# Kernel optimization log

Measured on AMD Instinct MI355X. Metric: run time of the kernel, lower is better.

## Reference

```python
import jax, jax.numpy as jnp
import numpy as np
import math

H_SP, W_SP = 200, 200          # BEV spatial shape (single level, m == h)
D_MODEL = 256
N_HEADS = 8
N_POINTS = 4
D_HEAD = D_MODEL // N_HEADS


def _grid_init_bias():
    # Matches TemporalSelfAttention._reset_parameters for sampling_offsets.bias
    thetas = np.arange(N_HEADS, dtype=np.float32) * (2.0 * np.pi / N_HEADS)
    grid = np.stack([np.cos(thetas), np.sin(thetas)], -1)
    grid = grid / np.abs(grid).max(-1, keepdims=True)
    grid = np.tile(grid[:, None, None, :], (1, 1, N_POINTS, 1))  # (NH, 1, P, 2)
    for i in range(N_POINTS):
        grid[:, :, i, :] *= (i + 1)
    return jnp.asarray(grid.reshape(-1), dtype=jnp.float32)


def setup_inputs() -> dict:
    key = jax.random.key(0)
    ks = jax.random.split(key, 10)
    N = 1
    Lq = H_SP * W_SP
    Lin = H_SP * W_SP
    xav = math.sqrt(6.0 / (2 * D_MODEL))
    query = jax.random.normal(ks[0], (N, Lq, D_MODEL), jnp.float32)
    query_pos = jax.random.normal(ks[1], (N, Lq, D_MODEL), jnp.float32)
    reference_points = jax.random.uniform(ks[2], (N, Lq, 1, 2), jnp.float32)
    input_flatten = jax.random.normal(ks[3], (N, Lin, D_MODEL), jnp.float32)
    W_value = jax.random.uniform(ks[4], (D_MODEL, D_MODEL), jnp.float32, -xav, xav)
    b_value = jnp.zeros((D_MODEL,), jnp.float32)
    # small random weights (trained-model-like) + canonical grid bias
    W_off = jax.random.normal(ks[5], (N_HEADS * N_POINTS * 2, D_MODEL), jnp.float32) * 0.005
    b_off = _grid_init_bias()
    W_attn = jax.random.normal(ks[6], (N_HEADS * N_POINTS, D_MODEL), jnp.float32) * 0.02
    b_attn = jnp.zeros((N_HEADS * N_POINTS,), jnp.float32)
    W_out = jax.random.uniform(ks[7], (D_MODEL, D_MODEL), jnp.float32, -xav, xav)
    b_out = jnp.zeros((D_MODEL,), jnp.float32)
    return dict(query=query, query_pos=query_pos, reference_points=reference_points,
                input_flatten=input_flatten, W_value=W_value, b_value=b_value,
                W_off=W_off, b_off=b_off, W_attn=W_attn, b_attn=b_attn,
                W_out=W_out, b_out=b_out)


def _bilinear_sample(vflat, x, y):
    # vflat: (N, NH, H*W, DH); x, y: (N, NH, K) pixel coords (align_corners=False)
    # Zero padding outside the feature map, matching the MSDeformAttn CUDA kernel.
    x0f = jnp.floor(x)
    y0f = jnp.floor(y)
    x0 = x0f.astype(jnp.int32)
    y0 = y0f.astype(jnp.int32)
    lw = x - x0f
    lh = y - y0f
    gather = jax.vmap(jax.vmap(lambda v, i: v[i]))  # over batch, head
    acc = jnp.zeros(x.shape + (vflat.shape[-1],), vflat.dtype)
    corners = ((y0, x0, (1.0 - lh) * (1.0 - lw)),
               (y0, x0 + 1, (1.0 - lh) * lw),
               (y0 + 1, x0, lh * (1.0 - lw)),
               (y0 + 1, x0 + 1, lh * lw))
    for yi, xi, wgt in corners:
        valid = ((xi >= 0) & (xi < W_SP) & (yi >= 0) & (yi < H_SP)).astype(vflat.dtype)
        idx = jnp.clip(yi, 0, H_SP - 1) * W_SP + jnp.clip(xi, 0, W_SP - 1)
        g = gather(vflat, idx)                      # (N, NH, K, DH)
        acc = acc + (wgt * valid)[..., None] * g
    return acc


def reference(query, query_pos, reference_points, input_flatten,
              W_value, b_value, W_off, b_off, W_attn, b_attn, W_out, b_out):
    N, Lq, _ = query.shape
    q = query + query_pos
    value = input_flatten @ W_value.T + b_value                     # (N, Lin, D)
    value = value.reshape(N, -1, N_HEADS, D_HEAD).transpose(0, 2, 1, 3)  # (N, NH, Lin, DH)
    off = (q @ W_off.T + b_off).reshape(N, Lq, N_HEADS, N_POINTS, 2)
    attn = jax.nn.softmax((q @ W_attn.T + b_attn).reshape(N, Lq, N_HEADS, N_POINTS), axis=-1)
    norm = jnp.array([W_SP, H_SP], jnp.float32)                      # offset_normalizer (w, h)
    ref = reference_points[:, :, 0, :][:, :, None, None, :]          # (N, Lq, 1, 1, 2)
    loc = ref + off / norm                                           # (N, Lq, NH, P, 2) in [0,1]
    x = (loc[..., 0] * W_SP - 0.5).transpose(0, 2, 1, 3).reshape(N, N_HEADS, Lq * N_POINTS)
    y = (loc[..., 1] * H_SP - 0.5).transpose(0, 2, 1, 3).reshape(N, N_HEADS, Lq * N_POINTS)
    sampled = _bilinear_sample(value, x, y).reshape(N, N_HEADS, Lq, N_POINTS, D_HEAD)
    out = jnp.einsum('nhqpd,nqhp->nqhd', sampled, attn).reshape(N, Lq, D_MODEL)
    return out @ W_out.T + b_out
```

## Files before the change

kernel.cpp:

```cpp
#include <hip/hip_runtime.h>
#include <math.h>

#define LQ 40000
#define DMODEL 256
#define NHD 8
#define NPT 4
#define DHD 32
#define HSP 200
#define WSP 200

typedef short s16x8 __attribute__((ext_vector_type(8)));
typedef float f32x4 __attribute__((ext_vector_type(4)));

__device__ __forceinline__ unsigned short f2b(float f) {
    unsigned u = __builtin_bit_cast(unsigned, f);
    u += 0x7FFFu + ((u >> 16) & 1u);
    return (unsigned short)(u >> 16);
}
__device__ __forceinline__ float b2f(unsigned short u) {
    return __builtin_bit_cast(float, ((unsigned)u) << 16);
}

template <typename AT, typename CT, bool HasA2>
__global__ __launch_bounds__(256) void gemm_mfma(
    const AT* __restrict__ A, const float* __restrict__ A2,
    const float* __restrict__ W1, const float* __restrict__ b1,
    const float* __restrict__ W2, const float* __restrict__ b2,
    int split, int ncols, CT* __restrict__ C, int ldC)
{
    constexpr int LDA = 264;
    __shared__ __align__(16) unsigned short Asm[64 * LDA];
    __shared__ __align__(16) unsigned short Bsm[64 * LDA];

    const int t = threadIdx.x;
    const int rowBase = blockIdx.x * 64;
    const int colBase = blockIdx.y * 64;

#pragma unroll
    for (int rep = 0; rep < 8; ++rep) {
        int f8 = t + 256 * rep;
        int row = f8 >> 5;
        int c8 = f8 & 31;
        unsigned short* dst = &Asm[row * LDA + c8 * 8];
        if constexpr (sizeof(AT) == 4) {
            const float* Ap = (const float*)A + (size_t)(rowBase + row) * 256 + c8 * 8;
            float4 v0 = *(const float4*)Ap;
            float4 v1 = *(const float4*)(Ap + 4);
            if constexpr (HasA2) {
                const float* Bp = A2 + (size_t)(rowBase + row) * 256 + c8 * 8;
                float4 w0 = *(const float4*)Bp;
                float4 w1 = *(const float4*)(Bp + 4);
                v0.x += w0.x; v0.y += w0.y; v0.z += w0.z; v0.w += w0.w;
                v1.x += w1.x; v1.y += w1.y; v1.z += w1.z; v1.w += w1.w;
            }
            union { unsigned short u[8]; uint4 v; } tmp;
            tmp.u[0] = f2b(v0.x); tmp.u[1] = f2b(v0.y);
            tmp.u[2] = f2b(v0.z); tmp.u[3] = f2b(v0.w);
            tmp.u[4] = f2b(v1.x); tmp.u[5] = f2b(v1.y);
            tmp.u[6] = f2b(v1.z); tmp.u[7] = f2b(v1.w);
            *(uint4*)dst = tmp.v;
        } else {
            const unsigned short* Ap =
                (const unsigned short*)A + (size_t)(rowBase + row) * 256 + c8 * 8;
            *(uint4*)dst = *(const uint4*)Ap;
        }
    }

#pragma unroll
    for (int rep = 0; rep < 8; ++rep) {
        int f8 = t + 256 * rep;
        int row = f8 >> 5;
        int c8 = f8 & 31;
        int n = colBase + row;
        int nc = n < ncols ? n : (ncols - 1);
        const float* Wp = (nc < split) ? (W1 + (size_t)nc * 256)
                                       : (W2 + (size_t)(nc - split) * 256);
        float4 v0 = *(const float4*)(Wp + c8 * 8);
        float4 v1 = *(const float4*)(Wp + c8 * 8 + 4);
        union { unsigned short u[8]; uint4 v; } tmp;
        tmp.u[0] = f2b(v0.x); tmp.u[1] = f2b(v0.y);
        tmp.u[2] = f2b(v0.z); tmp.u[3] = f2b(v0.w);
        tmp.u[4] = f2b(v1.x); tmp.u[5] = f2b(v1.y);
        tmp.u[6] = f2b(v1.z); tmp.u[7] = f2b(v1.w);
        *(uint4*)&Bsm[row * LDA + c8 * 8] = tmp.v;
    }

    __syncthreads();

    const int wave = t >> 6;
    const int lane = t & 63;
    const int l15 = lane & 15;
    const int quad = lane >> 4;

    f32x4 acc[4];
#pragma unroll
    for (int m = 0; m < 4; ++m) acc[m] = (f32x4){0.f, 0.f, 0.f, 0.f};

#pragma unroll
    for (int ks = 0; ks < 8; ++ks) {
        s16x8 bfrag = *(const s16x8*)&Bsm[(wave * 16 + l15) * LDA + ks * 32 + quad * 8];
#pragma unroll
        for (int m = 0; m < 4; ++m) {
            s16x8 afrag = *(const s16x8*)&Asm[(m * 16 + l15) * LDA + ks * 32 + quad * 8];
            acc[m] = __builtin_amdgcn_mfma_f32_16x16x32_bf16(afrag, bfrag, acc[m], 0, 0, 0);
        }
    }

    const int col = colBase + wave * 16 + l15;
    if (col < ncols) {
        float bb = (col < split) ? b1[col] : b2[col - split];
#pragma unroll
        for (int m = 0; m < 4; ++m)
#pragma unroll
            for (int r2 = 0; r2 < 4; ++r2) {
                int row = rowBase + m * 16 + quad * 4 + r2;
                float v = acc[m][r2] + bb;
                if constexpr (sizeof(CT) == 2)
                    C[(size_t)row * ldC + col] = (CT)f2b(v);
                else
                    C[(size_t)row * ldC + col] = (CT)v;
            }
    }
}

__global__ __launch_bounds__(256) void sample_kernel(
    const float* __restrict__ raw, const float* __restrict__ rp,
    const unsigned short* __restrict__ value, unsigned short* __restrict__ outa)
{
    __shared__ int4   sIdx[8][8][4];
    __shared__ float4 sW[8][8][4];

    const int t = threadIdx.x;
    {
        const int qi = t >> 5, h = (t >> 2) & 7, p = t & 3;
        const int q = blockIdx.x * 8 + qi;
        const float* r = raw + (size_t)q * 96;
        float l0 = r[64 + h * 4 + 0], l1 = r[64 + h * 4 + 1];
        float l2 = r[64 + h * 4 + 2], l3 = r[64 + h * 4 + 3];
        float mx = fmaxf(fmaxf(l0, l1), fmaxf(l2, l3));
        float e0 = __expf(l0 - mx), e1 = __expf(l1 - mx);
        float e2 = __expf(l2 - mx), e3 = __expf(l3 - mx);
        float inv = 1.f / (e0 + e1 + e2 + e3);
        float ep = (p == 0) ? e0 : (p == 1) ? e1 : (p == 2) ? e2 : e3;
        float wp = ep * inv;

        float x = rp[(size_t)q * 2 + 0] * (float)WSP - 0.5f + r[h * 8 + p * 2 + 0];
        float y = rp[(size_t)q * 2 + 1] * (float)HSP - 0.5f + r[h * 8 + p * 2 + 1];
        float x0f = floorf(x), y0f = floorf(y);
        int x0 = (int)x0f, y0 = (int)y0f;
        float lw = x - x0f, lh = y - y0f;
        float cw[4] = {(1.f - lh) * (1.f - lw), (1.f - lh) * lw,
                       lh * (1.f - lw), lh * lw};
        int4 I; float4 W;
        int* Ip = &I.x; float* Wp = &W.x;
#pragma unroll
        for (int c = 0; c < 4; ++c) {
            int cx = x0 + (c & 1), cy = y0 + (c >> 1);
            bool valid = (cx >= 0) & (cx < WSP) & (cy >= 0) & (cy < HSP);
            int ccx = cx < 0 ? 0 : (cx > WSP - 1 ? WSP - 1 : cx);
            int ccy = cy < 0 ? 0 : (cy > HSP - 1 ? HSP - 1 : cy);
            Ip[c] = (ccy * WSP + ccx) * DMODEL + h * DHD;
            Wp[c] = valid ? cw[c] * wp : 0.f;
        }
        sIdx[qi][h][p] = I;
        sW[qi][h][p] = W;
    }
    __syncthreads();

    const int h = t >> 5, d = t & 31;
    for (int qi = 0; qi < 8; ++qi) {
        float acc = 0.f;
#pragma unroll
        for (int p = 0; p < 4; ++p) {
            int4 I = sIdx[qi][h][p];
            float4 W = sW[qi][h][p];
            acc += W.x * b2f(value[I.x + d]);
            acc += W.y * b2f(value[I.y + d]);
            acc += W.z * b2f(value[I.z + d]);
            acc += W.w * b2f(value[I.w + d]);
        }
        int q = blockIdx.x * 8 + qi;
        outa[(size_t)q * DMODEL + h * DHD + d] = f2b(acc);
    }
}

extern "C" void kernel_launch(void* const* d_in, const int* in_sizes, int n_in,
                              void* d_out, int out_size, void* d_ws, size_t ws_size,
                              hipStream_t stream)
{
    const float* query         = (const float*)d_in[0];
    const float* query_pos     = (const float*)d_in[1];
    const float* ref_points    = (const float*)d_in[2];
    const float* input_flatten = (const float*)d_in[3];
    const float* W_value       = (const float*)d_in[4];
    const float* b_value       = (const float*)d_in[5];
    const float* W_off         = (const float*)d_in[6];
    const float* b_off         = (const float*)d_in[7];
    const float* W_attn        = (const float*)d_in[8];
    const float* b_attn        = (const float*)d_in[9];
    const float* W_out         = (const float*)d_in[10];
    const float* b_out         = (const float*)d_in[11];
    float* out = (float*)d_out;

    unsigned short* val  = (unsigned short*)d_ws;
    float*          raw  = (float*)(val + (size_t)LQ * DMODEL);
    unsigned short* outa = (unsigned short*)(raw + (size_t)LQ * 96);

    dim3 blk(256);

    gemm_mfma<float, unsigned short, false><<<dim3(LQ / 64, 4), blk, 0, stream>>>(
        input_flatten, nullptr, W_value, b_value, W_value, b_value, 256, 256,
        val, DMODEL);

    gemm_mfma<float, float, true><<<dim3(LQ / 64, 2), blk, 0, stream>>>(
        query, query_pos, W_off, b_off, W_attn, b_attn, 64, 96, raw, 96);

    sample_kernel<<<dim3(LQ / 8), blk, 0, stream>>>(raw, ref_points, val, outa);

    gemm_mfma<unsigned short, float, false><<<dim3(LQ / 64, 4), blk, 0, stream>>>(
        outa, nullptr, W_out, b_out, W_out, b_out, 256, 256, out, DMODEL);
}
```

Baseline: 287.0 us.

## Pre-convert weights to bf16 and compute full output width per GEMM block

```diff
diff --git a/kernel.cpp b/kernel.cpp
--- a/kernel.cpp
+++ b/kernel.cpp
@@ -21,105 +21,127 @@
     return __builtin_bit_cast(float, ((unsigned)u) << 16);
 }
 
-template <typename AT, typename CT, bool HasA2>
+__global__ __launch_bounds__(256) void convert_weights(
+    const float* __restrict__ s0, const float* __restrict__ s1,
+    const float* __restrict__ s2, const float* __restrict__ s3,
+    unsigned short* __restrict__ dst)
+{
+    int i4 = (blockIdx.x * 256 + threadIdx.x) * 4;
+    const float* src;
+    int base;
+    if (i4 < 65536)       { src = s0; base = 0; }
+    else if (i4 < 81920)  { src = s1; base = 65536; }
+    else if (i4 < 90112)  { src = s2; base = 81920; }
+    else                  { src = s3; base = 90112; }
+    float4 v = *(const float4*)(src + (i4 - base));
+    union { unsigned short u[4]; uint2 q; } tmp;
+    tmp.u[0] = f2b(v.x); tmp.u[1] = f2b(v.y);
+    tmp.u[2] = f2b(v.z); tmp.u[3] = f2b(v.w);
+    *(uint2*)(dst + i4) = tmp.q;
+}
+
+template <int NCOLS, typename AT, typename CT, bool HasA2>
 __global__ __launch_bounds__(256) void gemm_mfma(
     const AT* __restrict__ A, const float* __restrict__ A2,
-    const float* __restrict__ W1, const float* __restrict__ b1,
-    const float* __restrict__ W2, const float* __restrict__ b2,
-    int split, int ncols, CT* __restrict__ C, int ldC)
-{
-    constexpr int LDA = 264;
-    __shared__ __align__(16) unsigned short Asm[64 * LDA];
-    __shared__ __align__(16) unsigned short Bsm[64 * LDA];
+    const unsigned short* __restrict__ Wb,
+    const float* __restrict__ b1, const float* __restrict__ b2, int split,
+    CT* __restrict__ C)
+{
+    constexpr int NT = NCOLS / 16;
+    constexpr int JMAX = (NT + 3) / 4;
+    constexpr int PITCH = 72;
+    __shared__ __align__(16) unsigned short As[64 * PITCH];
+    __shared__ __align__(16) unsigned short Bs[NCOLS * PITCH];
 
     const int t = threadIdx.x;
-    const int rowBase = blockIdx.x * 64;
-    const int colBase = blockIdx.y * 64;
-
-#pragma unroll
-    for (int rep = 0; rep < 8; ++rep) {
-        int f8 = t + 256 * rep;
-        int row = f8 >> 5;
-        int c8 = f8 & 31;
-        unsigned short* dst = &Asm[row * LDA + c8 * 8];
-        if constexpr (sizeof(AT) == 4) {
-            const float* Ap = (const float*)A + (size_t)(rowBase + row) * 256 + c8 * 8;
-            float4 v0 = *(const float4*)Ap;
-            float4 v1 = *(const float4*)(Ap + 4);
-            if constexpr (HasA2) {
-                const float* Bp = A2 + (size_t)(rowBase + row) * 256 + c8 * 8;
-                float4 w0 = *(const float4*)Bp;
-                float4 w1 = *(const float4*)(Bp + 4);
-                v0.x += w0.x; v0.y += w0.y; v0.z += w0.z; v0.w += w0.w;
-                v1.x += w1.x; v1.y += w1.y; v1.z += w1.z; v1.w += w1.w;
+    const int wave = t >> 6, lane = t & 63;
+    const int l15 = lane & 15, quad = lane >> 4;
+    const size_t rowBase = (size_t)blockIdx.x * 64;
+
+    f32x4 acc[4][JMAX];
+#pragma unroll
+    for (int m = 0; m < 4; ++m)
+#pragma unroll
+        for (int j = 0; j < JMAX; ++j) acc[m][j] = (f32x4){0.f, 0.f, 0.f, 0.f};
+
+    for (int k0 = 0; k0 < 256; k0 += 64) {
+        if (k0) __syncthreads();
+#pragma unroll
+        for (int rep = 0; rep < 2; ++rep) {
+            int f8 = t + 256 * rep;
+            int row = f8 >> 3, g = f8 & 7;
+            unsigned short* dst = &As[row * PITCH + g * 8];
+            if constexpr (sizeof(AT) == 4) {
+                const float* Ap = (const float*)A + (rowBase + row) * 256 + k0 + g * 8;
+                float4 v0 = *(const float4*)Ap;
+                float4 v1 = *(const float4*)(Ap + 4);
+                if constexpr (HasA2) {
+                    const float* Bp = A2 + (rowBase + row) * 256 + k0 + g * 8;
+                    float4 w0 = *(const float4*)Bp;
+                    float4 w1 = *(const float4*)(Bp + 4);
+                    v0.x += w0.x; v0.y += w0.y; v0.z += w0.z; v0.w += w0.w;
+                    v1.x += w1.x; v1.y += w1.y; v1.z += w1.z; v1.w += w1.w;
+                }
+                union { unsigned short u[8]; uint4 v; } tmp;
+                tmp.u[0] = f2b(v0.x); tmp.u[1] = f2b(v0.y);
+                tmp.u[2] = f2b(v0.z); tmp.u[3] = f2b(v0.w);
+                tmp.u[4] = f2b(v1.x); tmp.u[5] = f2b(v1.y);
+                tmp.u[6] = f2b(v1.z); tmp.u[7] = f2b(v1.w);
+                *(uint4*)dst = tmp.v;
+            } else {
+                const unsigned short* Ap =
+                    (const unsigned short*)A + (rowBase + row) * 256 + k0 + g * 8;
+                *(uint4*)dst = *(const uint4*)Ap;
             }
-            union { unsigned short u[8]; uint4 v; } tmp;
-            tmp.u[0] = f2b(v0.x); tmp.u[1] = f2b(v0.y);
-            tmp.u[2] = f2b(v0.z); tmp.u[3] = f2b(v0.w);
-            tmp.u[4] = f2b(v1.x); tmp.u[5] = f2b(v1.y);
-            tmp.u[6] = f2b(v1.z); tmp.u[7] = f2b(v1.w);
-            *(uint4*)dst = tmp.v;
-        } else {
-            const unsigned short* Ap =
-                (const unsigned short*)A + (size_t)(rowBase + row) * 256 + c8 * 8;
-            *(uint4*)dst = *(const uint4*)Ap;
-        }
-    }
-
-#pragma unroll
-    for (int rep = 0; rep < 8; ++rep) {
-        int f8 = t + 256 * rep;
-        int row = f8 >> 5;
-        int c8 = f8 & 31;
-        int n = colBase + row;
-        int nc = n < ncols ? n : (ncols - 1);
-        const float* Wp = (nc < split) ? (W1 + (size_t)nc * 256)
-                                       : (W2 + (size_t)(nc - split) * 256);
-        float4 v0 = *(const float4*)(Wp + c8 * 8);
-        float4 v1 = *(const float4*)(Wp + c8 * 8 + 4);
-        union { unsigned short u[8]; uint4 v; } tmp;
-        tmp.u[0] = f2b(v0.x); tmp.u[1] = f2b(v0.y);
-        tmp.u[2] = f2b(v0.z); tmp.u[3] = f2b(v0.w);
-        tmp.u[4] = f2b(v1.x); tmp.u[5] = f2b(v1.y);
-        tmp.u[6] = f2b(v1.z); tmp.u[7] = f2b(v1.w);
-        *(uint4*)&Bsm[row * LDA + c8 * 8] = tmp.v;
-    }
-
-    __syncthreads();
-
-    const int wave = t >> 6;
-    const int lane = t & 63;
-    const int l15 = lane & 15;
-    const int quad = lane >> 4;
-
-    f32x4 acc[4];
-#pragma unroll
-    for (int m = 0; m < 4; ++m) acc[m] = (f32x4){0.f, 0.f, 0.f, 0.f};
-
-#pragma unroll
-    for (int ks = 0; ks < 8; ++ks) {
-        s16x8 bfrag = *(const s16x8*)&Bsm[(wave * 16 + l15) * LDA + ks * 32 + quad * 8];
-#pragma unroll
-        for (int m = 0; m < 4; ++m) {
-            s16x8 afrag = *(const s16x8*)&Asm[(m * 16 + l15) * LDA + ks * 32 + quad * 8];
-            acc[m] = __builtin_amdgcn_mfma_f32_16x16x32_bf16(afrag, bfrag, acc[m], 0, 0, 0);
-        }
-    }
-
-    const int col = colBase + wave * 16 + l15;
-    if (col < ncols) {
-        float bb = (col < split) ? b1[col] : b2[col - split];
-#pragma unroll
-        for (int m = 0; m < 4; ++m)
-#pragma unroll
-            for (int r2 = 0; r2 < 4; ++r2) {
-                int row = rowBase + m * 16 + quad * 4 + r2;
-                float v = acc[m][r2] + bb;
-                if constexpr (sizeof(CT) == 2)
-                    C[(size_t)row * ldC + col] = (CT)f2b(v);
-                else
-                    C[(size_t)row * ldC + col] = (CT)v;
+        }
+#pragma unroll
+        for (int rep = 0; rep < NCOLS / 32; ++rep) {
+            int f8 = t + 256 * rep;
+            int row = f8 >> 3, g = f8 & 7;
+            *(uint4*)&Bs[row * PITCH + g * 8] =
+                *(const uint4*)&Wb[(size_t)row * 256 + k0 + g * 8];
+        }
+        __syncthreads();
+#pragma unroll
+        for (int ks = 0; ks < 2; ++ks) {
+            s16x8 a[4], b[JMAX];
+#pragma unroll
+            for (int m = 0; m < 4; ++m)
+                a[m] = *(const s16x8*)&As[(m * 16 + l15) * PITCH + ks * 32 + quad * 8];
+#pragma unroll
+            for (int j = 0; j < JMAX; ++j) {
+                int tl = wave + 4 * j;
+                if (tl < NT)
+                    b[j] = *(const s16x8*)&Bs[(tl * 16 + l15) * PITCH + ks * 32 + quad * 8];
             }
+#pragma unroll
+            for (int m = 0; m < 4; ++m)
+#pragma unroll
+                for (int j = 0; j < JMAX; ++j)
+                    if (wave + 4 * j < NT)
+                        acc[m][j] = __builtin_amdgcn_mfma_f32_16x16x32_bf16(
+                            a[m], b[j], acc[m][j], 0, 0, 0);
+        }
+    }
+
+#pragma unroll
+    for (int j = 0; j < JMAX; ++j) {
+        int tl = wave + 4 * j;
+        if (tl < NT) {
+            int col = tl * 16 + l15;
+            float bb = (col < split) ? b1[col] : b2[col - split];
+#pragma unroll
+            for (int m = 0; m < 4; ++m)
+#pragma unroll
+                for (int r2 = 0; r2 < 4; ++r2) {
+                    size_t row = rowBase + m * 16 + quad * 4 + r2;
+                    float v = acc[m][j][r2] + bb;
+                    if constexpr (sizeof(CT) == 2)
+                        C[row * NCOLS + col] = (CT)f2b(v);
+                    else
+                        C[row * NCOLS + col] = (CT)v;
+                }
+        }
     }
 }
 
@@ -130,10 +152,12 @@
     __shared__ int4   sIdx[8][8][4];
     __shared__ float4 sW[8][8][4];
 
+    const int b = blockIdx.x;
+    const int qb = (b & 7) * 625 + (b >> 3);
     const int t = threadIdx.x;
     {
         const int qi = t >> 5, h = (t >> 2) & 7, p = t & 3;
-        const int q = blockIdx.x * 8 + qi;
+        const int q = qb * 8 + qi;
         const float* r = raw + (size_t)q * 96;
         float l0 = r[64 + h * 4 + 0], l1 = r[64 + h * 4 + 1];
         float l2 = r[64 + h * 4 + 2], l3 = r[64 + h * 4 + 3];
@@ -179,7 +203,7 @@
             acc += W.z * b2f(value[I.z + d]);
             acc += W.w * b2f(value[I.w + d]);
         }
-        int q = blockIdx.x * 8 + qi;
+        int q = qb * 8 + qi;
         outa[(size_t)q * DMODEL + h * DHD + d] = f2b(acc);
     }
 }
@@ -205,18 +229,24 @@
     unsigned short* val  = (unsigned short*)d_ws;
     float*          raw  = (float*)(val + (size_t)LQ * DMODEL);
     unsigned short* outa = (unsigned short*)(raw + (size_t)LQ * 96);
+    unsigned short* wbuf = outa + (size_t)LQ * DMODEL;
+    unsigned short* wv   = wbuf;
+    unsigned short* woa  = wbuf + 65536;
+    unsigned short* wout = wbuf + 90112;
 
     dim3 blk(256);
 
-    gemm_mfma<float, unsigned short, false><<<dim3(LQ / 64, 4), blk, 0, stream>>>(
-        input_flatten, nullptr, W_value, b_value, W_value, b_value, 256, 256,
-        val, DMODEL);
-
-    gemm_mfma<float, float, true><<<dim3(LQ / 64, 2), blk, 0, stream>>>(
-        query, query_pos, W_off, b_off, W_attn, b_attn, 64, 96, raw, 96);
+    convert_weights<<<dim3(152), blk, 0, stream>>>(
+        W_value, W_off, W_attn, W_out, wbuf);
+
+    gemm_mfma<256, float, unsigned short, false><<<dim3(LQ / 64), blk, 0, stream>>>(
+        input_flatten, nullptr, wv, b_value, b_value, 256, val);
+
+    gemm_mfma<96, float, float, true><<<dim3(LQ / 64), blk, 0, stream>>>(
+        query, query_pos, woa, b_off, b_attn, 64, raw);
 
     sample_kernel<<<dim3(LQ / 8), blk, 0, stream>>>(raw, ref_points, val, outa);
 
-    gemm_mfma<unsigned short, float, false><<<dim3(LQ / 64, 4), blk, 0, stream>>>(
-        outa, nullptr, W_out, b_out, W_out, b_out, 256, 256, out, DMODEL);
-}
+    gemm_mfma<256, unsigned short, float, false><<<dim3(LQ / 64), blk, 0, stream>>>(
+        outa, nullptr, wout, b_out, b_out, 256, out);
+}
```

Measured after the change: 281.9 us. Within noise of the previous version (-1.8%).

## Restructure GEMMs to full-width row tiles and use head-major value layout

Applied to the files above, without the earlier changes.

```diff
diff --git a/kernel.cpp b/kernel.cpp
--- a/kernel.cpp
+++ b/kernel.cpp
@@ -20,106 +20,116 @@
 __device__ __forceinline__ float b2f(unsigned short u) {
     return __builtin_bit_cast(float, ((unsigned)u) << 16);
 }
-
-template <typename AT, typename CT, bool HasA2>
-__global__ __launch_bounds__(256) void gemm_mfma(
+__device__ __forceinline__ unsigned short pk8(const float4& v0, const float4& v1,
+                                              unsigned short* o) {
+    o[0] = f2b(v0.x); o[1] = f2b(v0.y); o[2] = f2b(v0.z); o[3] = f2b(v0.w);
+    o[4] = f2b(v1.x); o[5] = f2b(v1.y); o[6] = f2b(v1.z); o[7] = f2b(v1.w);
+    return 0;
+}
+
+template <int NCOLS, int TPW, typename AT, bool HasA2, int CMODE>
+__global__ __launch_bounds__(256, 2) void gemm_mfma(
     const AT* __restrict__ A, const float* __restrict__ A2,
     const float* __restrict__ W1, const float* __restrict__ b1,
-    const float* __restrict__ W2, const float* __restrict__ b2,
-    int split, int ncols, CT* __restrict__ C, int ldC)
+    const float* __restrict__ W2, const float* __restrict__ b2, int split,
+    void* __restrict__ Cv)
 {
-    constexpr int LDA = 264;
-    __shared__ __align__(16) unsigned short Asm[64 * LDA];
-    __shared__ __align__(16) unsigned short Bsm[64 * LDA];
+    constexpr int NT = NCOLS / 16;
+    __shared__ __align__(16) unsigned short As[64 * 256];
 
     const int t = threadIdx.x;
-    const int rowBase = blockIdx.x * 64;
-    const int colBase = blockIdx.y * 64;
-
+    const int wave = t >> 6, lane = t & 63;
+    const int l15 = lane & 15, quad = lane >> 4;
+    const size_t rowBase = (size_t)blockIdx.x * 64;
+
+    float4 sv0[8], sv1[8];
+    uint4  sb[8];
 #pragma unroll
     for (int rep = 0; rep < 8; ++rep) {
-        int f8 = t + 256 * rep;
-        int row = f8 >> 5;
-        int c8 = f8 & 31;
-        unsigned short* dst = &Asm[row * LDA + c8 * 8];
+        int fb = rep * 4 + wave;
+        int m = fb & 3, ks = fb >> 2;
+        size_t src = (rowBase + m * 16 + l15) * 256 + ks * 32 + quad * 8;
         if constexpr (sizeof(AT) == 4) {
-            const float* Ap = (const float*)A + (size_t)(rowBase + row) * 256 + c8 * 8;
-            float4 v0 = *(const float4*)Ap;
-            float4 v1 = *(const float4*)(Ap + 4);
+            const float* Ap = (const float*)A + src;
+            sv0[rep] = *(const float4*)Ap;
+            sv1[rep] = *(const float4*)(Ap + 4);
             if constexpr (HasA2) {
-                const float* Bp = A2 + (size_t)(rowBase + row) * 256 + c8 * 8;
+                const float* Bp = A2 + src;
                 float4 w0 = *(const float4*)Bp;
                 float4 w1 = *(const float4*)(Bp + 4);
-                v0.x += w0.x; v0.y += w0.y; v0.z += w0.z; v0.w += w0.w;
-                v1.x += w1.x; v1.y += w1.y; v1.z += w1.z; v1.w += w1.w;
+                sv0[rep].x += w0.x; sv0[rep].y += w0.y;
+                sv0[rep].z += w0.z; sv0[rep].w += w0.w;
+                sv1[rep].x += w1.x; sv1[rep].y += w1.y;
+                sv1[rep].z += w1.z; sv1[rep].w += w1.w;
             }
+        } else {
+            sb[rep] = *(const uint4*)((const unsigned short*)A + src);
+        }
+    }
+
+    s16x8 bf[TPW][8];
+#pragma unroll
+    for (int j = 0; j < TPW; ++j) {
+        int c = wave + 4 * j;
+        if (c < NT) {
+            int col = c * 16 + l15;
+            const float* Wp = (col < split) ? (W1 + (size_t)col * 256)
+                                            : (W2 + (size_t)(col - split) * 256);
+#pragma unroll
+            for (int ks = 0; ks < 8; ++ks) {
+                float4 w0 = *(const float4*)(Wp + ks * 32 + quad * 8);
+                float4 w1 = *(const float4*)(Wp + ks * 32 + quad * 8 + 4);
+                union { unsigned short u[8]; s16x8 v; } tmp;
+                pk8(w0, w1, tmp.u);
+                bf[j][ks] = tmp.v;
+            }
+        }
+    }
+
+#pragma unroll
+    for (int rep = 0; rep < 8; ++rep) {
+        int fb = rep * 4 + wave;
+        unsigned short* dst = &As[(fb * 64 + lane) * 8];
+        if constexpr (sizeof(AT) == 4) {
             union { unsigned short u[8]; uint4 v; } tmp;
-            tmp.u[0] = f2b(v0.x); tmp.u[1] = f2b(v0.y);
-            tmp.u[2] = f2b(v0.z); tmp.u[3] = f2b(v0.w);
-            tmp.u[4] = f2b(v1.x); tmp.u[5] = f2b(v1.y);
-            tmp.u[6] = f2b(v1.z); tmp.u[7] = f2b(v1.w);
+            pk8(sv0[rep], sv1[rep], tmp.u);
             *(uint4*)dst = tmp.v;
         } else {
-            const unsigned short* Ap =
-                (const unsigned short*)A + (size_t)(rowBase + row) * 256 + c8 * 8;
-            *(uint4*)dst = *(const uint4*)Ap;
-        }
-    }
-
-#pragma unroll
-    for (int rep = 0; rep < 8; ++rep) {
-        int f8 = t + 256 * rep;
-        int row = f8 >> 5;
-        int c8 = f8 & 31;
-        int n = colBase + row;
-        int nc = n < ncols ? n : (ncols - 1);
-        const float* Wp = (nc < split) ? (W1 + (size_t)nc * 256)
-                                       : (W2 + (size_t)(nc - split) * 256);
-        float4 v0 = *(const float4*)(Wp + c8 * 8);
-        float4 v1 = *(const float4*)(Wp + c8 * 8 + 4);
-        union { unsigned short u[8]; uint4 v; } tmp;
-        tmp.u[0] = f2b(v0.x); tmp.u[1] = f2b(v0.y);
-        tmp.u[2] = f2b(v0.z); tmp.u[3] = f2b(v0.w);
-        tmp.u[4] = f2b(v1.x); tmp.u[5] = f2b(v1.y);
-        tmp.u[6] = f2b(v1.z); tmp.u[7] = f2b(v1.w);
-        *(uint4*)&Bsm[row * LDA + c8 * 8] = tmp.v;
-    }
-
+            *(uint4*)dst = sb[rep];
+        }
+    }
     __syncthreads();
 
-    const int wave = t >> 6;
-    const int lane = t & 63;
-    const int l15 = lane & 15;
-    const int quad = lane >> 4;
-
-    f32x4 acc[4];
-#pragma unroll
-    for (int m = 0; m < 4; ++m) acc[m] = (f32x4){0.f, 0.f, 0.f, 0.f};
-
-#pragma unroll
-    for (int ks = 0; ks < 8; ++ks) {
-        s16x8 bfrag = *(const s16x8*)&Bsm[(wave * 16 + l15) * LDA + ks * 32 + quad * 8];
-#pragma unroll
-        for (int m = 0; m < 4; ++m) {
-            s16x8 afrag = *(const s16x8*)&Asm[(m * 16 + l15) * LDA + ks * 32 + quad * 8];
-            acc[m] = __builtin_amdgcn_mfma_f32_16x16x32_bf16(afrag, bfrag, acc[m], 0, 0, 0);
-        }
-    }
-
-    const int col = colBase + wave * 16 + l15;
-    if (col < ncols) {
-        float bb = (col < split) ? b1[col] : b2[col - split];
-#pragma unroll
-        for (int m = 0; m < 4; ++m)
-#pragma unroll
-            for (int r2 = 0; r2 < 4; ++r2) {
-                int row = rowBase + m * 16 + quad * 4 + r2;
-                float v = acc[m][r2] + bb;
-                if constexpr (sizeof(CT) == 2)
-                    C[(size_t)row * ldC + col] = (CT)f2b(v);
-                else
-                    C[(size_t)row * ldC + col] = (CT)v;
+#pragma unroll
+    for (int m = 0; m < 4; ++m) {
+        s16x8 a[8];
+#pragma unroll
+        for (int ks = 0; ks < 8; ++ks)
+            a[ks] = *(const s16x8*)&As[(((ks << 2) | m) * 64 + lane) * 8];
+#pragma unroll
+        for (int j = 0; j < TPW; ++j) {
+            int c = wave + 4 * j;
+            if (c < NT) {
+                f32x4 acc = (f32x4){0.f, 0.f, 0.f, 0.f};
+#pragma unroll
+                for (int ks = 0; ks < 8; ++ks)
+                    acc = __builtin_amdgcn_mfma_f32_16x16x32_bf16(a[ks], bf[j][ks],
+                                                                  acc, 0, 0, 0);
+                int col = c * 16 + l15;
+                float bb = (col < split) ? b1[col] : b2[col - split];
+#pragma unroll
+                for (int r2 = 0; r2 < 4; ++r2) {
+                    size_t row = rowBase + m * 16 + quad * 4 + r2;
+                    float v = acc[r2] + bb;
+                    if constexpr (CMODE == 1) {
+                        ((unsigned short*)Cv)[(((size_t)(c >> 1) * LQ + row) << 5)
+                                              + ((c & 1) << 4) + l15] = f2b(v);
+                    } else {
+                        ((float*)Cv)[row * NCOLS + col] = v;
+                    }
+                }
             }
+        }
     }
 }
 
@@ -159,7 +169,7 @@
             bool valid = (cx >= 0) & (cx < WSP) & (cy >= 0) & (cy < HSP);
             int ccx = cx < 0 ? 0 : (cx > WSP - 1 ? WSP - 1 : cx);
             int ccy = cy < 0 ? 0 : (cy > HSP - 1 ? HSP - 1 : cy);
-            Ip[c] = (ccy * WSP + ccx) * DMODEL + h * DHD;
+            Ip[c] = (ccy * WSP + ccx) * DHD;
             Wp[c] = valid ? cw[c] * wp : 0.f;
         }
         sIdx[qi][h][p] = I;
@@ -167,20 +177,41 @@
     }
     __syncthreads();
 
-    const int h = t >> 5, d = t & 31;
-    for (int qi = 0; qi < 8; ++qi) {
-        float acc = 0.f;
+    const int qq = t >> 6, h = (t >> 3) & 7, d8 = t & 7;
+    const unsigned short* vp = value + (size_t)h * LQ * DHD + d8 * 4;
+#pragma unroll
+    for (int e = 0; e < 2; ++e) {
+        int qi = qq * 2 + e;
+        float a0 = 0.f, a1 = 0.f, a2 = 0.f, a3 = 0.f;
 #pragma unroll
         for (int p = 0; p < 4; ++p) {
             int4 I = sIdx[qi][h][p];
             float4 W = sW[qi][h][p];
-            acc += W.x * b2f(value[I.x + d]);
-            acc += W.y * b2f(value[I.y + d]);
-            acc += W.z * b2f(value[I.z + d]);
-            acc += W.w * b2f(value[I.w + d]);
+            uint2 g0 = *(const uint2*)(vp + I.x);
+            uint2 g1 = *(const uint2*)(vp + I.y);
+            uint2 g2 = *(const uint2*)(vp + I.z);
+            uint2 g3 = *(const uint2*)(vp + I.w);
+            a0 += W.x * b2f((unsigned short)g0.x);
+            a1 += W.x * b2f((unsigned short)(g0.x >> 16));
+            a2 += W.x * b2f((unsigned short)g0.y);
+            a3 += W.x * b2f((unsigned short)(g0.y >> 16));
+            a0 += W.y * b2f((unsigned short)g1.x);
+            a1 += W.y * b2f((unsigned short)(g1.x >> 16));
+            a2 += W.y * b2f((unsigned short)g1.y);
+            a3 += W.y * b2f((unsigned short)(g1.y >> 16));
+            a0 += W.z * b2f((unsigned short)g2.x);
+            a1 += W.z * b2f((unsigned short)(g2.x >> 16));
+            a2 += W.z * b2f((unsigned short)g2.y);
+            a3 += W.z * b2f((unsigned short)(g2.y >> 16));
+            a0 += W.w * b2f((unsigned short)g3.x);
+            a1 += W.w * b2f((unsigned short)(g3.x >> 16));
+            a2 += W.w * b2f((unsigned short)g3.y);
+            a3 += W.w * b2f((unsigned short)(g3.y >> 16));
         }
         int q = blockIdx.x * 8 + qi;
-        outa[(size_t)q * DMODEL + h * DHD + d] = f2b(acc);
+        union { unsigned short u[4]; uint2 v; } o;
+        o.u[0] = f2b(a0); o.u[1] = f2b(a1); o.u[2] = f2b(a2); o.u[3] = f2b(a3);
+        *(uint2*)&outa[(size_t)q * DMODEL + h * DHD + d8 * 4] = o.v;
     }
 }
 
@@ -208,15 +239,14 @@
 
     dim3 blk(256);
 
-    gemm_mfma<float, unsigned short, false><<<dim3(LQ / 64, 4), blk, 0, stream>>>(
-        input_flatten, nullptr, W_value, b_value, W_value, b_value, 256, 256,
-        val, DMODEL);
-
-    gemm_mfma<float, float, true><<<dim3(LQ / 64, 2), blk, 0, stream>>>(
-        query, query_pos, W_off, b_off, W_attn, b_attn, 64, 96, raw, 96);
+    gemm_mfma<256, 4, float, false, 1><<<dim3(LQ / 64), blk, 0, stream>>>(
+        input_flatten, nullptr, W_value, b_value, W_value, b_value, 256, val);
+
+    gemm_mfma<96, 2, float, true, 0><<<dim3(LQ / 64), blk, 0, stream>>>(
+        query, query_pos, W_off, b_off, W_attn, b_attn, 64, raw);
 
     sample_kernel<<<dim3(LQ / 8), blk, 0, stream>>>(raw, ref_points, val, outa);
 
-    gemm_mfma<unsigned short, float, false><<<dim3(LQ / 64, 4), blk, 0, stream>>>(
-        outa, nullptr, W_out, b_out, W_out, b_out, 256, 256, out, DMODEL);
-}
+    gemm_mfma<256, 4, unsigned short, false, 0><<<dim3(LQ / 64), blk, 0, stream>>>(
+        outa, nullptr, W_out, b_out, W_out, b_out, 256, out);
+}
```

Result: slower. 298.8 us (+4.1%).
